# Optimization experiments

Hardware: AMD Instinct MI355X
Metric: run time of the kernel (lower is better)

Reference implementation:

```python
import jax, jax.numpy as jnp
import numpy as np
import math

D = 1024
H = 16
DH = D // H
B, S = 4, 2048
EPS = 1e-5

def _layernorm(x, g, b):
    mu = jnp.mean(x, axis=-1, keepdims=True)
    var = jnp.mean((x - mu) ** 2, axis=-1, keepdims=True)
    return (x - mu) * jax.lax.rsqrt(var + EPS) * g + b

def setup_inputs() -> dict:
    key = jax.random.key(0)
    ks = jax.random.split(key, 12)
    s = 1.0 / math.sqrt(D)
    s4 = 1.0 / math.sqrt(4 * D)
    return {
        "embed": jax.random.normal(ks[0], (B, S, D), jnp.float32),
        "src_mask": jnp.zeros((S, S), jnp.float32),
        # torch Linear weights are [out, in]
        "Wk": jax.random.uniform(ks[1], (D, D), jnp.float32, -s, s),
        "Wq": jax.random.uniform(ks[2], (D, D), jnp.float32, -s, s),
        "Wv": jax.random.uniform(ks[3], (D, D), jnp.float32, -s, s),
        "w1": jax.random.uniform(ks[4], (4 * D, D), jnp.float32, -s, s),
        "b1": jax.random.uniform(ks[5], (4 * D,), jnp.float32, -s, s),
        "w2": jax.random.uniform(ks[6], (D, 4 * D), jnp.float32, -s4, s4),
        "b2": jax.random.uniform(ks[7], (D,), jnp.float32, -s4, s4),
        "g1": jnp.ones((D,), jnp.float32),
        "be1": jnp.zeros((D,), jnp.float32),
        "g2": jnp.ones((D,), jnp.float32),
        "be2": jnp.zeros((D,), jnp.float32),
    }

def reference(embed, src_mask, Wk, Wq, Wv, w1, b1, w2, b2, g1, be1, g2, be2):
    # projections: x @ W.T, then split heads -> [B, H, S, DH]
    def proj(W):
        return jnp.einsum('bsd,ed->bse', embed, W).reshape(B, S, H, DH).transpose(0, 2, 1, 3)
    q, k, v = proj(Wq), proj(Wk), proj(Wv)
    # NOTE: mask added BEFORE the 1/sqrt(d_per_h) scaling (as in the source)
    scores = (jnp.einsum('bhqd,bhkd->bhqk', q, k) + src_mask[None, None]) / math.sqrt(DH)
    attn = jax.nn.softmax(scores, axis=-1)
    o = jnp.einsum('bhqk,bhkd->bhqd', attn, v)  # [B, H, S, DH]
    o = o.transpose(0, 2, 1, 3).reshape(B, S, D)
    out = _layernorm(o + embed, g1, be1)
    ff = jnp.einsum('bsf,df->bsd', jax.nn.relu(jnp.einsum('bsd,fd->bsf', out, w1) + b1), w2) + b2
    return _layernorm(ff + out, g2, be2)
```

## Files before the change

### kernel.cpp

```cpp
#include <hip/hip_runtime.h>

typedef unsigned short u16;
typedef unsigned int u32;
typedef __attribute__((ext_vector_type(8))) __bf16 bf16x8;
typedef __attribute__((ext_vector_type(4))) float f32x4;
typedef __attribute__((ext_vector_type(16))) float f32x16;
typedef __attribute__((ext_vector_type(2))) unsigned u32x2;

#define DEV static __device__ __forceinline__

DEV u16 f2bf(float x) {
  union { float f; u32 u; } c; c.f = x;
  u32 r = c.u + 0x7FFFu + ((c.u >> 16) & 1u);
  return (u16)(r >> 16);
}
DEV float bf2f(u16 u) {
  union { u32 u; float f; } c; c.u = ((u32)u) << 16;
  return c.f;
}
DEV u32 cvtpk(float lo, float hi) {
  u32 r;
  asm("v_cvt_pk_bf16_f32 %0, %1, %2" : "=v"(r) : "v"(lo), "v"(hi));
  return r;
}

DEV void gll16(const void* g, void* l) {
  __builtin_amdgcn_global_load_lds(
      (__attribute__((address_space(1))) void*)(g),
      (__attribute__((address_space(3))) void*)(l), 16, 0, 0);
}

__global__ void k_cvt(const float* __restrict__ src, u16* __restrict__ dst, int n4,
                      float scale) {
  int i = blockIdx.x * blockDim.x + threadIdx.x;
  int stride = gridDim.x * blockDim.x;
  for (; i < n4; i += stride) {
    float4 v = reinterpret_cast<const float4*>(src)[i];
    ushort4 o;
    o.x = f2bf(v.x * scale); o.y = f2bf(v.y * scale);
    o.z = f2bf(v.z * scale); o.w = f2bf(v.w * scale);
    reinterpret_cast<ushort4*>(dst)[i] = o;
  }
}

enum { EPI_BF16 = 0, EPI_VT = 1, EPI_RELU_BF16 = 2, EPI_F32 = 3 };

template <int EPI>
__global__ __launch_bounds__(256, 2) void k_gemm(
    const u16* __restrict__ A, const u16* __restrict__ B,
    const float* __restrict__ bias, void* __restrict__ Cout,
    int M, int N, int K) {
  __shared__ u16 As[128][32];
  __shared__ u16 Bs[128][32];
  const int tid = threadIdx.x;
  const int w = tid >> 6, l = tid & 63;
  const int fr = l & 15, fq = l >> 4;
  const int wm = (w >> 1) << 6, wn = (w & 1) << 6;
  const int m0 = blockIdx.y << 7, n0 = blockIdx.x << 7;
  const int sr = tid >> 2;
  const int sc = (tid & 3) << 3;
  const u16* Ag = A + (size_t)(m0 + sr) * K + sc;
  const u16* Bg = B + (size_t)(n0 + sr) * K + sc;
  const u16* Ag2 = Ag + (size_t)64 * K;
  const u16* Bg2 = Bg + (size_t)64 * K;
  u16* AsB0 = &As[w << 4][0];
  u16* AsB1 = &As[64 + (w << 4)][0];
  u16* BsB0 = &Bs[w << 4][0];
  u16* BsB1 = &Bs[64 + (w << 4)][0];

  f32x4 acc[4][4] = {};
  for (int k0 = 0; k0 < K; k0 += 32) {
    __syncthreads();
    gll16(Ag + k0, AsB0);
    gll16(Ag2 + k0, AsB1);
    gll16(Bg + k0, BsB0);
    gll16(Bg2 + k0, BsB1);
    __syncthreads();
    bf16x8 af[4], bfm[4];
#pragma unroll
    for (int i = 0; i < 4; ++i)
      af[i] = *reinterpret_cast<const bf16x8*>(&As[wm + i * 16 + fr][fq << 3]);
#pragma unroll
    for (int i = 0; i < 4; ++i)
      bfm[i] = *reinterpret_cast<const bf16x8*>(&Bs[wn + i * 16 + fr][fq << 3]);
#pragma unroll
    for (int i = 0; i < 4; ++i)
#pragma unroll
      for (int j = 0; j < 4; ++j)
        acc[i][j] = __builtin_amdgcn_mfma_f32_16x16x32_bf16(af[i], bfm[j], acc[i][j], 0, 0, 0);
  }

#pragma unroll
  for (int i = 0; i < 4; ++i) {
    const int rbase = m0 + wm + i * 16 + (fq << 2);
#pragma unroll
    for (int j = 0; j < 4; ++j) {
      const int col = n0 + wn + j * 16 + fr;
      float bv = 0.f;
      if (EPI == EPI_RELU_BF16 || EPI == EPI_F32) bv = bias[col];
#pragma unroll
      for (int r = 0; r < 4; ++r) {
        const int row = rbase + r;
        float v = acc[i][j][r];
        if (EPI == EPI_RELU_BF16) v = fmaxf(v + bv, 0.f);
        if (EPI == EPI_F32) v = v + bv;
        if (EPI == EPI_BF16 || EPI == EPI_RELU_BF16) {
          ((u16*)Cout)[(size_t)row * N + col] = f2bf(v);
        } else if (EPI == EPI_F32) {
          ((float*)Cout)[(size_t)row * N + col] = v;
        } else {
          const int bb = row >> 11, s = row & 2047;
          const int hh = col >> 6, dh = col & 63;
          ((u16*)Cout)[(size_t)((((bb << 4) + hh) << 6) | dh) * 2048 + s] = f2bf(v);
        }
      }
    }
  }
}

__global__ __launch_bounds__(256, 3) void k_attn(
    const u16* __restrict__ Q, const u16* __restrict__ Kb,
    const u16* __restrict__ Vt, u16* __restrict__ O) {
  __shared__ u16 sm[2][8192];
  const int tid = threadIdx.x;
  const int wq = tid >> 6;
  const int l = tid & 63;
  const int ql = l & 31;
  const int h = l >> 5;
  const int flat = blockIdx.y * 64 + blockIdx.x;
  const int xcd = flat & 7, mm = flat >> 3;
  const int bh = (xcd << 3) | (mm & 7);
  const int qb = mm >> 3;
  const int b = bh >> 4, hd = bh & 15;
  const int hcol = hd << 6;
  const int q0 = (b << 11) + (qb << 7) + (wq << 5);

  bf16x8 qf[4];
  {
    const u16* qptr = Q + (size_t)(q0 + ql) * 1024 + hcol + h * 8;
#pragma unroll
    for (int s = 0; s < 4; ++s)
      qf[s] = *reinterpret_cast<const bf16x8*>(qptr + s * 16);
  }
  const u16* kg = Kb + (size_t)(b << 11) * 1024 + hcol;
  const u16* vg = Vt + (size_t)(bh << 6) * 2048;
  const int wbase = tid & ~63;

  auto stage = [&](u16* buf, int kv0) {
#pragma unroll
    for (int j = 0; j < 2; ++j) {
      int p = j * 256 + tid;
      int r = p >> 3, c = (p & 7) ^ (r & 7);
      gll16(kg + (size_t)(kv0 + r) * 1024 + c * 8, buf + (j * 256 + wbase) * 8);
    }
#pragma unroll
    for (int j = 0; j < 2; ++j) {
      int p = j * 256 + tid;
      int r = p >> 3, c = (p & 7) ^ (r & 7);
      gll16(vg + (size_t)r * 2048 + kv0 + c * 8, buf + 4096 + (j * 256 + wbase) * 8);
    }
  };

  f32x16 o0 = {}, o1 = {};
  float ldn = 0.f;

  stage(sm[0], 0);
  __syncthreads();

  for (int it = 0; it < 32; ++it) {
    const u16* cur = sm[it & 1];
    if (it < 31) stage(sm[(it + 1) & 1], (it + 1) << 6);

    const u16* smK = cur;
    const u16* smV = cur + 4096;
    f32x16 st0 = {}, st1 = {};
#pragma unroll
    for (int s = 0; s < 4; ++s) {
      const int c = ((s << 1) + h) ^ (ql & 7);
      bf16x8 kf0 = *reinterpret_cast<const bf16x8*>(smK + ((ql << 3) + c) * 8);
      bf16x8 kf1 = *reinterpret_cast<const bf16x8*>(smK + (((32 + ql) << 3) + c) * 8);
      st0 = __builtin_amdgcn_mfma_f32_32x32x16_bf16(kf0, qf[s], st0, 0, 0, 0);
      st1 = __builtin_amdgcn_mfma_f32_32x32x16_bf16(kf1, qf[s], st1, 0, 0, 0);
    }

    float rsum = 0.f;
#pragma unroll
    for (int r = 0; r < 16; ++r) {
      st0[r] = __builtin_amdgcn_exp2f(st0[r]);
      st1[r] = __builtin_amdgcn_exp2f(st1[r]);
      rsum += st0[r] + st1[r];
    }
    ldn += rsum;

#pragma unroll
    for (int t = 0; t < 2; ++t) {
      f32x16& st = t ? st1 : st0;
      u32 a = cvtpk(st[0], st[1]);
      u32 bq = cvtpk(st[4], st[5]);
      u32 c2 = cvtpk(st[2], st[3]);
      u32 d = cvtpk(st[6], st[7]);
      u32x2 s02 = __builtin_amdgcn_permlane32_swap(a, bq, false, false);
      u32x2 s13 = __builtin_amdgcn_permlane32_swap(c2, d, false, false);
      union { u32 w[4]; bf16x8 v; } f0;
      f0.w[0] = s02[0]; f0.w[1] = s13[0]; f0.w[2] = s02[1]; f0.w[3] = s13[1];
      u32 e = cvtpk(st[8], st[9]);
      u32 f = cvtpk(st[12], st[13]);
      u32 g = cvtpk(st[10], st[11]);
      u32 hh = cvtpk(st[14], st[15]);
      u32x2 s02b = __builtin_amdgcn_permlane32_swap(e, f, false, false);
      u32x2 s13b = __builtin_amdgcn_permlane32_swap(g, hh, false, false);
      union { u32 w[4]; bf16x8 v; } f1;
      f1.w[0] = s02b[0]; f1.w[1] = s13b[0]; f1.w[2] = s02b[1]; f1.w[3] = s13b[1];

      const int ca = ((t << 2) + h) ^ (ql & 7);
      const int cb = ((t << 2) + 2 + h) ^ (ql & 7);
      bf16x8 v0a = *reinterpret_cast<const bf16x8*>(smV + ((ql << 3) + ca) * 8);
      bf16x8 v0b = *reinterpret_cast<const bf16x8*>(smV + ((ql << 3) + cb) * 8);
      bf16x8 v1a = *reinterpret_cast<const bf16x8*>(smV + (((32 + ql) << 3) + ca) * 8);
      bf16x8 v1b = *reinterpret_cast<const bf16x8*>(smV + (((32 + ql) << 3) + cb) * 8);
      o0 = __builtin_amdgcn_mfma_f32_32x32x16_bf16(f0.v, v0a, o0, 0, 0, 0);
      o0 = __builtin_amdgcn_mfma_f32_32x32x16_bf16(f1.v, v0b, o0, 0, 0, 0);
      o1 = __builtin_amdgcn_mfma_f32_32x32x16_bf16(f0.v, v1a, o1, 0, 0, 0);
      o1 = __builtin_amdgcn_mfma_f32_32x32x16_bf16(f1.v, v1b, o1, 0, 0, 0);
    }
    __syncthreads();
  }

  ldn += __shfl_xor(ldn, 32);
  float inv = 1.f / ldn;
#pragma unroll
  for (int r = 0; r < 16; ++r) {
    float iv = __shfl(inv, (r & 3) + 8 * (r >> 2) + (h << 2));
    int row = q0 + (r & 3) + 8 * (r >> 2) + (h << 2);
    O[(size_t)row * 1024 + hcol + ql] = f2bf(o0[r] * iv);
    O[(size_t)row * 1024 + hcol + 32 + ql] = f2bf(o1[r] * iv);
  }
}

template <bool IN1_BF16, bool RESID_BF16, bool WRITE_F32, bool WRITE_BF16>
__global__ __launch_bounds__(256) void k_ln(
    const void* __restrict__ in1, const void* __restrict__ resid,
    const float* __restrict__ gamma, const float* __restrict__ beta,
    float* __restrict__ outf, u16* __restrict__ outb) {
  const int row = blockIdx.x;
  const int t = threadIdx.x;
  float v[4];
  {
    float a0, a1, a2, a3, r0, r1, r2, r3;
    if (IN1_BF16) {
      ushort4 a = reinterpret_cast<const ushort4*>((const u16*)in1 + (size_t)row * 1024)[t];
      a0 = bf2f(a.x); a1 = bf2f(a.y); a2 = bf2f(a.z); a3 = bf2f(a.w);
    } else {
      float4 a = reinterpret_cast<const float4*>((const float*)in1 + (size_t)row * 1024)[t];
      a0 = a.x; a1 = a.y; a2 = a.z; a3 = a.w;
    }
    if (RESID_BF16) {
      ushort4 rr = reinterpret_cast<const ushort4*>((const u16*)resid + (size_t)row * 1024)[t];
      r0 = bf2f(rr.x); r1 = bf2f(rr.y); r2 = bf2f(rr.z); r3 = bf2f(rr.w);
    } else {
      float4 rr = reinterpret_cast<const float4*>((const float*)resid + (size_t)row * 1024)[t];
      r0 = rr.x; r1 = rr.y; r2 = rr.z; r3 = rr.w;
    }
    v[0] = a0 + r0; v[1] = a1 + r1; v[2] = a2 + r2; v[3] = a3 + r3;
  }
  float s = v[0] + v[1] + v[2] + v[3];
  float ss = v[0] * v[0] + v[1] * v[1] + v[2] * v[2] + v[3] * v[3];
#pragma unroll
  for (int m = 1; m < 64; m <<= 1) {
    s += __shfl_xor(s, m);
    ss += __shfl_xor(ss, m);
  }
  __shared__ float red[2][4];
  const int w = t >> 6, l = t & 63;
  if (l == 0) { red[0][w] = s; red[1][w] = ss; }
  __syncthreads();
  s = red[0][0] + red[0][1] + red[0][2] + red[0][3];
  ss = red[1][0] + red[1][1] + red[1][2] + red[1][3];
  const float mu = s * (1.f / 1024.f);
  const float var = ss * (1.f / 1024.f) - mu * mu;
  const float rstd = rsqrtf(var + 1e-5f);
  float4 g = reinterpret_cast<const float4*>(gamma)[t];
  float4 bb = reinterpret_cast<const float4*>(beta)[t];
  float y0 = (v[0] - mu) * rstd * g.x + bb.x;
  float y1 = (v[1] - mu) * rstd * g.y + bb.y;
  float y2 = (v[2] - mu) * rstd * g.z + bb.z;
  float y3 = (v[3] - mu) * rstd * g.w + bb.w;
  if (WRITE_F32) {
    float4 yo; yo.x = y0; yo.y = y1; yo.z = y2; yo.w = y3;
    reinterpret_cast<float4*>(outf + (size_t)row * 1024)[t] = yo;
  }
  if (WRITE_BF16) {
    ushort4 o;
    o.x = f2bf(y0); o.y = f2bf(y1); o.z = f2bf(y2); o.w = f2bf(y3);
    reinterpret_cast<ushort4*>(outb + (size_t)row * 1024)[t] = o;
  }
}

extern "C" void kernel_launch(void* const* d_in, const int* in_sizes, int n_in,
                              void* d_out, int out_size, void* d_ws, size_t ws_size,
                              hipStream_t stream) {
  const float* embed = (const float*)d_in[0];
  const float* Wk = (const float*)d_in[2];
  const float* Wq = (const float*)d_in[3];
  const float* Wv = (const float*)d_in[4];
  const float* w1 = (const float*)d_in[5];
  const float* b1 = (const float*)d_in[6];
  const float* w2 = (const float*)d_in[7];
  const float* b2 = (const float*)d_in[8];
  const float* g1 = (const float*)d_in[9];
  const float* be1 = (const float*)d_in[10];
  const float* g2 = (const float*)d_in[11];
  const float* be2 = (const float*)d_in[12];

  char* ws = (char*)d_ws;
  const size_t MB = 1ull << 20;
  u16* Xb   = (u16*)(ws + 0);
  u16* Wqb  = (u16*)(ws + 16 * MB);
  u16* Wkb  = (u16*)(ws + 18 * MB);
  u16* Wvb  = (u16*)(ws + 20 * MB);
  u16* w1b  = (u16*)(ws + 22 * MB);
  u16* w2b  = (u16*)(ws + 22 * MB);
  u16* Qb   = (u16*)(ws + 30 * MB);
  u16* Kbb  = (u16*)(ws + 46 * MB);
  u16* Vtb  = (u16*)(ws + 62 * MB);
  u16* Ob   = (u16*)(ws + 78 * MB);
  u16* x1b  = (u16*)(ws + 0);
  u16* hb   = (u16*)(ws + 30 * MB);
  float* outp = (float*)d_out;

  auto cvt = [&](const float* s, u16* d, int n, float scale) {
    int n4 = n >> 2;
    int grid = (n4 + 255) / 256;
    if (grid > 2048) grid = 2048;
    k_cvt<<<dim3(grid), dim3(256), 0, stream>>>(s, d, n4, scale);
  };
  const float SC = 0.18033688011112042f;
  cvt(embed, Xb, 8192 * 1024, 1.f);
  cvt(Wq, Wqb, 1024 * 1024, SC);
  cvt(Wk, Wkb, 1024 * 1024, 1.f);
  cvt(Wv, Wvb, 1024 * 1024, 1.f);
  cvt(w1, w1b, 4096 * 1024, 1.f);

  k_gemm<EPI_BF16><<<dim3(8, 64), 256, 0, stream>>>(Xb, Wqb, nullptr, Qb, 8192, 1024, 1024);
  k_gemm<EPI_BF16><<<dim3(8, 64), 256, 0, stream>>>(Xb, Wkb, nullptr, Kbb, 8192, 1024, 1024);
  k_gemm<EPI_VT><<<dim3(8, 64), 256, 0, stream>>>(Xb, Wvb, nullptr, Vtb, 8192, 1024, 1024);

  k_attn<<<dim3(64, 16), 256, 0, stream>>>(Qb, Kbb, Vtb, Ob);

  k_ln<true, false, false, true><<<dim3(8192), 256, 0, stream>>>(
      Ob, embed, g1, be1, nullptr, x1b);

  k_gemm<EPI_RELU_BF16><<<dim3(32, 64), 256, 0, stream>>>(x1b, w1b, b1, hb, 8192, 4096, 1024);

  cvt(w2, w2b, 1024 * 4096, 1.f);

  k_gemm<EPI_F32><<<dim3(8, 64), 256, 0, stream>>>(hb, w2b, b2, outp, 8192, 1024, 4096);

  k_ln<false, true, true, false><<<dim3(8192), 256, 0, stream>>>(
      outp, x1b, g2, be2, outp, nullptr);
}
```

Baseline: 401.2 us.

## Rewrite GEMMs with 256x256 double-buffered tiles, fused QKV, split-K FFN2

Replaces the 128x128 single-buffered GEMM with a 512-thread, 256x256-tile kernel. It uses double-buffered swizzled LDS staging with explicit vmcnt waits, XCD-aware block remapping and raised MFMA priority. The Q/K/V projections are fused into one GEMM over a concatenated weight matrix. The second FFN GEMM is split along K into two partial outputs, reduced inside a new LayerNorm kernel that also adds the bias and residual. The attention loop gets the same finer-grained waitcnt/barrier and setprio treatment. The aim is more data reuse per tile, overlap of loads with MFMA, and fewer launches, at the cost of extra workspace and higher register/LDS pressure.

```diff
diff --git a/kernel.cpp b/kernel.cpp
--- a/kernel.cpp
+++ b/kernel.cpp
@@ -43,75 +43,123 @@
   }
 }
 
-enum { EPI_BF16 = 0, EPI_VT = 1, EPI_RELU_BF16 = 2, EPI_F32 = 3 };
+enum { EPI_QKV = 0, EPI_RELU = 1, EPI_F32OUT = 2 };
 
 template <int EPI>
-__global__ __launch_bounds__(256, 2) void k_gemm(
-    const u16* __restrict__ A, const u16* __restrict__ B,
-    const float* __restrict__ bias, void* __restrict__ Cout,
-    int M, int N, int K) {
-  __shared__ u16 As[128][32];
-  __shared__ u16 Bs[128][32];
+__global__ __launch_bounds__(512, 2) void k_gemm2(
+    const u16* __restrict__ A, int lda,
+    const u16* __restrict__ B, int ldb, int KLEN,
+    const float* __restrict__ bias,
+    void* __restrict__ C0, void* __restrict__ C1, int N) {
+  __shared__ u16 sm[2][32768];
   const int tid = threadIdx.x;
-  const int w = tid >> 6, l = tid & 63;
+  const int wid = tid >> 6, l = tid & 63;
   const int fr = l & 15, fq = l >> 4;
-  const int wm = (w >> 1) << 6, wn = (w & 1) << 6;
-  const int m0 = blockIdx.y << 7, n0 = blockIdx.x << 7;
-  const int sr = tid >> 2;
-  const int sc = (tid & 3) << 3;
-  const u16* Ag = A + (size_t)(m0 + sr) * K + sc;
-  const u16* Bg = B + (size_t)(n0 + sr) * K + sc;
-  const u16* Ag2 = Ag + (size_t)64 * K;
-  const u16* Bg2 = Bg + (size_t)64 * K;
-  u16* AsB0 = &As[w << 4][0];
-  u16* AsB1 = &As[64 + (w << 4)][0];
-  u16* BsB0 = &Bs[w << 4][0];
-  u16* BsB1 = &Bs[64 + (w << 4)][0];
-
-  f32x4 acc[4][4] = {};
-  for (int k0 = 0; k0 < K; k0 += 32) {
-    __syncthreads();
-    gll16(Ag + k0, AsB0);
-    gll16(Ag2 + k0, AsB1);
-    gll16(Bg + k0, BsB0);
-    gll16(Bg2 + k0, BsB1);
-    __syncthreads();
-    bf16x8 af[4], bfm[4];
-#pragma unroll
-    for (int i = 0; i < 4; ++i)
-      af[i] = *reinterpret_cast<const bf16x8*>(&As[wm + i * 16 + fr][fq << 3]);
-#pragma unroll
-    for (int i = 0; i < 4; ++i)
-      bfm[i] = *reinterpret_cast<const bf16x8*>(&Bs[wn + i * 16 + fr][fq << 3]);
-#pragma unroll
-    for (int i = 0; i < 4; ++i)
-#pragma unroll
-      for (int j = 0; j < 4; ++j)
-        acc[i][j] = __builtin_amdgcn_mfma_f32_16x16x32_bf16(af[i], bfm[j], acc[i][j], 0, 0, 0);
-  }
-
-#pragma unroll
-  for (int i = 0; i < 4; ++i) {
-    const int rbase = m0 + wm + i * 16 + (fq << 2);
+  const int wm = wid >> 2, wn = wid & 3;
+  const int gx = gridDim.x, gy = gridDim.y;
+  const int nwg = gx * gy * gridDim.z;
+  const int lid = (blockIdx.z * gy + blockIdx.y) * gx + blockIdx.x;
+  const int rid = (lid & 7) * (nwg >> 3) + (lid >> 3);
+  const int bx = rid % gx;
+  const int t1 = rid / gx;
+  const int by = t1 % gy;
+  const int bz = t1 / gy;
+  const int m0 = by << 8, n0 = bx << 8;
+  const int kz = bz * KLEN;
+  const u16* Ag = A + (size_t)m0 * lda + kz;
+  const u16* Bg = B + (size_t)n0 * ldb + kz;
+
+  auto stage = [&](u16* buf, int k0) {
 #pragma unroll
     for (int j = 0; j < 4; ++j) {
-      const int col = n0 + wn + j * 16 + fr;
-      float bv = 0.f;
-      if (EPI == EPI_RELU_BF16 || EPI == EPI_F32) bv = bias[col];
-#pragma unroll
-      for (int r = 0; r < 4; ++r) {
-        const int row = rbase + r;
-        float v = acc[i][j][r];
-        if (EPI == EPI_RELU_BF16) v = fmaxf(v + bv, 0.f);
-        if (EPI == EPI_F32) v = v + bv;
-        if (EPI == EPI_BF16 || EPI == EPI_RELU_BF16) {
-          ((u16*)Cout)[(size_t)row * N + col] = f2bf(v);
-        } else if (EPI == EPI_F32) {
-          ((float*)Cout)[(size_t)row * N + col] = v;
+      int n = (j << 9) + tid;
+      int r = n >> 3, gs = (n & 7) ^ (r & 7);
+      gll16(Ag + (size_t)r * lda + k0 + (gs << 3),
+            buf + (size_t)((j << 9) + (wid << 6)) * 8);
+    }
+#pragma unroll
+    for (int j = 0; j < 4; ++j) {
+      int n = (j << 9) + tid;
+      int r = n >> 3, gs = (n & 7) ^ (r & 7);
+      gll16(Bg + (size_t)r * ldb + k0 + (gs << 3),
+            buf + 16384 + (size_t)((j << 9) + (wid << 6)) * 8);
+    }
+  };
+
+  f32x4 acc[8][4] = {};
+  const int NT = KLEN >> 6;
+  stage(sm[0], 0);
+  for (int t = 0; t < NT; ++t) {
+    if (t + 1 < NT) {
+      stage(sm[(t + 1) & 1], (t + 1) << 6);
+      asm volatile("s_waitcnt vmcnt(8)" ::: "memory");
+    } else {
+      asm volatile("s_waitcnt vmcnt(0)" ::: "memory");
+    }
+    __builtin_amdgcn_s_barrier();
+    const u16* As = sm[t & 1];
+    const u16* Bs = As + 16384;
+    __builtin_amdgcn_s_setprio(1);
+#pragma unroll
+    for (int s = 0; s < 2; ++s) {
+      bf16x8 bfm[4];
+#pragma unroll
+      for (int j = 0; j < 4; ++j) {
+        int rl = (wn << 6) + (j << 4) + fr;
+        int sl = ((s << 2) + fq) ^ (fr & 7);
+        bfm[j] = *reinterpret_cast<const bf16x8*>(Bs + (rl << 6) + (sl << 3));
+      }
+#pragma unroll
+      for (int i = 0; i < 8; ++i) {
+        int rl = (wm << 7) + (i << 4) + fr;
+        int sl = ((s << 2) + fq) ^ (fr & 7);
+        bf16x8 af = *reinterpret_cast<const bf16x8*>(As + (rl << 6) + (sl << 3));
+#pragma unroll
+        for (int j = 0; j < 4; ++j)
+          acc[i][j] = __builtin_amdgcn_mfma_f32_16x16x32_bf16(af, bfm[j], acc[i][j], 0, 0, 0);
+      }
+    }
+    __builtin_amdgcn_s_setprio(0);
+    __builtin_amdgcn_s_barrier();
+  }
+
+#pragma unroll
+  for (int i = 0; i < 8; ++i) {
+    const int rbase = m0 + (wm << 7) + (i << 4) + (fq << 2);
+#pragma unroll
+    for (int j = 0; j < 4; ++j) {
+      const int col = n0 + (wn << 6) + (j << 4) + fr;
+      if (EPI == EPI_RELU) {
+        const float bv = bias[col];
+#pragma unroll
+        for (int r = 0; r < 4; ++r)
+          ((u16*)C0)[(size_t)(rbase + r) * N + col] = f2bf(fmaxf(acc[i][j][r] + bv, 0.f));
+      } else if (EPI == EPI_F32OUT) {
+        float* C = bz ? (float*)C1 : (float*)C0;
+#pragma unroll
+        for (int r = 0; r < 4; ++r)
+          C[(size_t)(rbase + r) * N + col] = acc[i][j][r];
+      } else {
+        if (n0 < 1024) {
+          u16* Q = (u16*)C0;
+#pragma unroll
+          for (int r = 0; r < 4; ++r)
+            Q[(size_t)(rbase + r) * 1024 + col] = f2bf(acc[i][j][r]);
+        } else if (n0 < 2048) {
+          u16* Kp = (u16*)C0 + (8u << 20);
+#pragma unroll
+          for (int r = 0; r < 4; ++r)
+            Kp[(size_t)(rbase + r) * 1024 + (col - 1024)] = f2bf(acc[i][j][r]);
         } else {
-          const int bb = row >> 11, s = row & 2047;
-          const int hh = col >> 6, dh = col & 63;
-          ((u16*)Cout)[(size_t)((((bb << 4) + hh) << 6) | dh) * 2048 + s] = f2bf(v);
+          u16* Vp = (u16*)C0 + (16u << 20);
+          const int colv = col - 2048;
+          const int hh = colv >> 6, dh = colv & 63;
+          const int bb = rbase >> 11, s = rbase & 2047;
+          ushort4 o;
+          o.x = f2bf(acc[i][j][0]); o.y = f2bf(acc[i][j][1]);
+          o.z = f2bf(acc[i][j][2]); o.w = f2bf(acc[i][j][3]);
+          *reinterpret_cast<ushort4*>(
+              &Vp[(size_t)((((bb << 4) + hh) << 6) | dh) * 2048 + s]) = o;
         }
       }
     }
@@ -165,15 +213,20 @@
   float ldn = 0.f;
 
   stage(sm[0], 0);
-  __syncthreads();
 
   for (int it = 0; it < 32; ++it) {
-    const u16* cur = sm[it & 1];
-    if (it < 31) stage(sm[(it + 1) & 1], (it + 1) << 6);
-
-    const u16* smK = cur;
-    const u16* smV = cur + 4096;
+    if (it < 31) {
+      stage(sm[(it + 1) & 1], (it + 1) << 6);
+      asm volatile("s_waitcnt vmcnt(4)" ::: "memory");
+    } else {
+      asm volatile("s_waitcnt vmcnt(0)" ::: "memory");
+    }
+    __builtin_amdgcn_s_barrier();
+
+    const u16* smK = sm[it & 1];
+    const u16* smV = smK + 4096;
     f32x16 st0 = {}, st1 = {};
+    __builtin_amdgcn_s_setprio(1);
 #pragma unroll
     for (int s = 0; s < 4; ++s) {
       const int c = ((s << 1) + h) ^ (ql & 7);
@@ -182,6 +235,7 @@
       st0 = __builtin_amdgcn_mfma_f32_32x32x16_bf16(kf0, qf[s], st0, 0, 0, 0);
       st1 = __builtin_amdgcn_mfma_f32_32x32x16_bf16(kf1, qf[s], st1, 0, 0, 0);
     }
+    __builtin_amdgcn_s_setprio(0);
 
     float rsum = 0.f;
 #pragma unroll
@@ -192,6 +246,7 @@
     }
     ldn += rsum;
 
+    __builtin_amdgcn_s_setprio(1);
 #pragma unroll
     for (int t = 0; t < 2; ++t) {
       f32x16& st = t ? st1 : st0;
@@ -223,7 +278,8 @@
       o1 = __builtin_amdgcn_mfma_f32_32x32x16_bf16(f0.v, v1a, o1, 0, 0, 0);
       o1 = __builtin_amdgcn_mfma_f32_32x32x16_bf16(f1.v, v1b, o1, 0, 0, 0);
     }
-    __syncthreads();
+    __builtin_amdgcn_s_setprio(0);
+    __builtin_amdgcn_s_barrier();
   }
 
   ldn += __shfl_xor(ldn, 32);
@@ -271,8 +327,8 @@
     ss += __shfl_xor(ss, m);
   }
   __shared__ float red[2][4];
-  const int w = t >> 6, l = t & 63;
-  if (l == 0) { red[0][w] = s; red[1][w] = ss; }
+  const int w = t >> 6, ll = t & 63;
+  if (ll == 0) { red[0][w] = s; red[1][w] = ss; }
   __syncthreads();
   s = red[0][0] + red[0][1] + red[0][2] + red[0][3];
   ss = red[1][0] + red[1][1] + red[1][2] + red[1][3];
@@ -296,6 +352,54 @@
   }
 }
 
+template <bool SUM2>
+__global__ __launch_bounds__(256) void k_lnf(
+    const float* __restrict__ fA, const float* __restrict__ fB,
+    const float* __restrict__ b2, const u16* __restrict__ resid,
+    const float* __restrict__ gamma, const float* __restrict__ beta,
+    float* __restrict__ out) {
+  const int row = blockIdx.x;
+  const int t = threadIdx.x;
+  float v[4];
+  {
+    float4 a = reinterpret_cast<const float4*>(fA + (size_t)row * 1024)[t];
+    float4 bv = reinterpret_cast<const float4*>(b2)[t];
+    ushort4 rr = reinterpret_cast<const ushort4*>(resid + (size_t)row * 1024)[t];
+    v[0] = a.x + bv.x + bf2f(rr.x);
+    v[1] = a.y + bv.y + bf2f(rr.y);
+    v[2] = a.z + bv.z + bf2f(rr.z);
+    v[3] = a.w + bv.w + bf2f(rr.w);
+    if (SUM2) {
+      float4 c = reinterpret_cast<const float4*>(fB + (size_t)row * 1024)[t];
+      v[0] += c.x; v[1] += c.y; v[2] += c.z; v[3] += c.w;
+    }
+  }
+  float s = v[0] + v[1] + v[2] + v[3];
+  float ss = v[0] * v[0] + v[1] * v[1] + v[2] * v[2] + v[3] * v[3];
+#pragma unroll
+  for (int m = 1; m < 64; m <<= 1) {
+    s += __shfl_xor(s, m);
+    ss += __shfl_xor(ss, m);
+  }
+  __shared__ float red[2][4];
+  const int w = t >> 6, ll = t & 63;
+  if (ll == 0) { red[0][w] = s; red[1][w] = ss; }
+  __syncthreads();
+  s = red[0][0] + red[0][1] + red[0][2] + red[0][3];
+  ss = red[1][0] + red[1][1] + red[1][2] + red[1][3];
+  const float mu = s * (1.f / 1024.f);
+  const float var = ss * (1.f / 1024.f) - mu * mu;
+  const float rstd = rsqrtf(var + 1e-5f);
+  float4 g = reinterpret_cast<const float4*>(gamma)[t];
+  float4 bb = reinterpret_cast<const float4*>(beta)[t];
+  float4 yo;
+  yo.x = (v[0] - mu) * rstd * g.x + bb.x;
+  yo.y = (v[1] - mu) * rstd * g.y + bb.y;
+  yo.z = (v[2] - mu) * rstd * g.z + bb.z;
+  yo.w = (v[3] - mu) * rstd * g.w + bb.w;
+  reinterpret_cast<float4*>(out + (size_t)row * 1024)[t] = yo;
+}
+
 extern "C" void kernel_launch(void* const* d_in, const int* in_sizes, int n_in,
                               void* d_out, int out_size, void* d_ws, size_t ws_size,
                               hipStream_t stream) {
@@ -314,19 +418,17 @@
 
   char* ws = (char*)d_ws;
   const size_t MB = 1ull << 20;
-  u16* Xb   = (u16*)(ws + 0);
-  u16* Wqb  = (u16*)(ws + 16 * MB);
-  u16* Wkb  = (u16*)(ws + 18 * MB);
-  u16* Wvb  = (u16*)(ws + 20 * MB);
-  u16* w1b  = (u16*)(ws + 22 * MB);
-  u16* w2b  = (u16*)(ws + 22 * MB);
-  u16* Qb   = (u16*)(ws + 30 * MB);
-  u16* Kbb  = (u16*)(ws + 46 * MB);
-  u16* Vtb  = (u16*)(ws + 62 * MB);
-  u16* Ob   = (u16*)(ws + 78 * MB);
-  u16* x1b  = (u16*)(ws + 0);
-  u16* hb   = (u16*)(ws + 30 * MB);
+  u16* Xb    = (u16*)(ws + 0);
+  u16* Wqkvb = (u16*)(ws + 16 * MB);
+  u16* w1b   = (u16*)(ws + 22 * MB);
+  u16* w2b   = (u16*)(ws + 22 * MB);
+  u16* Qb    = (u16*)(ws + 30 * MB);
+  u16* Ob    = (u16*)(ws + 78 * MB);
+  u16* x1b   = (u16*)(ws + 0);
+  u16* hb    = (u16*)(ws + 30 * MB);
+  float* ffB = (float*)(ws + 94 * MB);
   float* outp = (float*)d_out;
+  const bool split = ws_size >= 126 * MB;
 
   auto cvt = [&](const float* s, u16* d, int n, float scale) {
     int n4 = n >> 2;
@@ -336,26 +438,32 @@
   };
   const float SC = 0.18033688011112042f;
   cvt(embed, Xb, 8192 * 1024, 1.f);
-  cvt(Wq, Wqb, 1024 * 1024, SC);
-  cvt(Wk, Wkb, 1024 * 1024, 1.f);
-  cvt(Wv, Wvb, 1024 * 1024, 1.f);
+  cvt(Wq, Wqkvb, 1024 * 1024, SC);
+  cvt(Wk, Wqkvb + (1u << 20), 1024 * 1024, 1.f);
+  cvt(Wv, Wqkvb + (2u << 20), 1024 * 1024, 1.f);
   cvt(w1, w1b, 4096 * 1024, 1.f);
 
-  k_gemm<EPI_BF16><<<dim3(8, 64), 256, 0, stream>>>(Xb, Wqb, nullptr, Qb, 8192, 1024, 1024);
-  k_gemm<EPI_BF16><<<dim3(8, 64), 256, 0, stream>>>(Xb, Wkb, nullptr, Kbb, 8192, 1024, 1024);
-  k_gemm<EPI_VT><<<dim3(8, 64), 256, 0, stream>>>(Xb, Wvb, nullptr, Vtb, 8192, 1024, 1024);
-
-  k_attn<<<dim3(64, 16), 256, 0, stream>>>(Qb, Kbb, Vtb, Ob);
+  k_gemm2<EPI_QKV><<<dim3(12, 32, 1), 512, 0, stream>>>(
+      Xb, 1024, Wqkvb, 1024, 1024, nullptr, Qb, nullptr, 0);
+
+  k_attn<<<dim3(64, 16), 256, 0, stream>>>(
+      Qb, Qb + (8u << 20), Qb + (16u << 20), Ob);
 
   k_ln<true, false, false, true><<<dim3(8192), 256, 0, stream>>>(
       Ob, embed, g1, be1, nullptr, x1b);
 
-  k_gemm<EPI_RELU_BF16><<<dim3(32, 64), 256, 0, stream>>>(x1b, w1b, b1, hb, 8192, 4096, 1024);
+  k_gemm2<EPI_RELU><<<dim3(16, 32, 1), 512, 0, stream>>>(
+      x1b, 1024, w1b, 1024, 1024, b1, hb, nullptr, 4096);
 
   cvt(w2, w2b, 1024 * 4096, 1.f);
 
-  k_gemm<EPI_F32><<<dim3(8, 64), 256, 0, stream>>>(hb, w2b, b2, outp, 8192, 1024, 4096);
-
-  k_ln<false, true, true, false><<<dim3(8192), 256, 0, stream>>>(
-      outp, x1b, g2, be2, outp, nullptr);
-}
+  if (split) {
+    k_gemm2<EPI_F32OUT><<<dim3(4, 32, 2), 512, 0, stream>>>(
+        hb, 4096, w2b, 4096, 2048, nullptr, outp, ffB, 1024);
+    k_lnf<true><<<dim3(8192), 256, 0, stream>>>(outp, ffB, b2, x1b, g2, be2, outp);
+  } else {
+    k_gemm2<EPI_F32OUT><<<dim3(4, 32, 1), 512, 0, stream>>>(
+        hb, 4096, w2b, 4096, 4096, nullptr, outp, nullptr, 1024);
+    k_lnf<false><<<dim3(8192), 256, 0, stream>>>(outp, nullptr, b2, x1b, g2, be2, outp);
+  }
+}
```

New measurement: 345.6 us. 1.16x faster.
